# Kernel tuning notes

Hardware: AMD Instinct MI355X
Metric: run time of the kernel (lower is better)

## Reference

```python
import jax, jax.numpy as jnp
import numpy as np

MARGIN = 0.3
LOSS_FLOOR = 1e-06


def setup_inputs() -> dict:
    key = jax.random.key(0)
    k1, k2 = jax.random.split(key)
    embeddings = jax.random.normal(k1, (8192, 128), dtype=jnp.float32)
    labels = jax.random.randint(k2, (8192,), 0, 512, dtype=jnp.int64)
    return {"embeddings": embeddings, "labels": labels}


def _pairwise_dist(x):
    # Euclidean cdist via the GEMM identity; clamp for numerical safety.
    sq = jnp.sum(x * x, axis=1)  # [N]
    d2 = sq[:, None] + sq[None, :] - 2.0 * (x @ x.T)  # [N, N]
    return jnp.sqrt(jnp.maximum(d2, 1e-12))


def reference(embeddings, labels):
    dist = _pairwise_dist(embeddings)  # [N, N]
    same = labels[None, :] == labels[:, None]  # [N, N]
    n = embeddings.shape[0]
    eye = jnp.eye(n, dtype=bool)
    mask_pos = same & ~eye
    mask_neg = ~same  # diagonal is same-label, so already excluded

    neg_inf = jnp.float32(-jnp.inf)
    pos_inf = jnp.float32(jnp.inf)
    hardest_pos = jnp.max(jnp.where(mask_pos, dist, neg_inf), axis=1)  # [N]
    hardest_neg = jnp.min(jnp.where(mask_neg, dist, pos_inf), axis=1)  # [N]

    valid = jnp.any(mask_pos, axis=1) & jnp.any(mask_neg, axis=1)  # [N]
    per_row = jnp.maximum(hardest_pos - hardest_neg + MARGIN, LOSS_FLOOR)
    num_valid = jnp.sum(valid)
    total = jnp.sum(jnp.where(valid, per_row, 0.0))
    return jnp.where(num_valid > 0, total / jnp.maximum(num_valid, 1), 0.0).astype(embeddings.dtype)
```

## Files before the change

kernel.cpp:

```cpp
#include <hip/hip_runtime.h>
#include <math.h>


#define NROWS 8192
#define DIM   128
#define JSPLIT 32
#define JCHUNK (NROWS / JSPLIT)
#define NSUB   4
#define SUBROWS 64

typedef short bf16x8 __attribute__((ext_vector_type(8)));
typedef float f32x4  __attribute__((ext_vector_type(4)));

static __device__ __forceinline__ unsigned short f2bf(float f) {
    unsigned u = __float_as_uint(f);
    unsigned r = (u + 0x7FFFu + ((u >> 16) & 1u)) >> 16;
    return (unsigned short)r;
}

static __device__ __forceinline__ unsigned encf(float f) {
    unsigned u = __float_as_uint(f);
    return (u & 0x80000000u) ? ~u : (u | 0x80000000u);
}
static __device__ __forceinline__ float decf(unsigned e) {
    unsigned u = (e & 0x80000000u) ? (e & 0x7FFFFFFFu) : ~e;
    return __uint_as_float(u);
}
#define ENC_PINF 0xFF800000u
#define ENC_NINF 0x007FFFFFu

static __device__ __forceinline__ void gload_lds16(const void* g, void* l) {
    __builtin_amdgcn_global_load_lds(
        (const __attribute__((address_space(1))) unsigned int*)g,
        (__attribute__((address_space(3))) unsigned int*)l, 16, 0, 0);
}

__global__ __launch_bounds__(256) void prep_kernel(
    const float* __restrict__ x, const int* __restrict__ labels,
    int* __restrict__ hist, float* __restrict__ sqp,
    float* __restrict__ sqh, unsigned* __restrict__ hpE,
    unsigned* __restrict__ hnE, unsigned short* __restrict__ xb) {
    int t = blockIdx.x * 256 + threadIdx.x;
    int row = t >> 5;
    int c = t & 31;
    float4 v = ((const float4*)x)[t];
    float ps = v.x * v.x + v.y * v.y + v.z * v.z + v.w * v.w;
#pragma unroll
    for (int s = 1; s < 32; s <<= 1) ps += __shfl_xor(ps, s, 64);
    if (c == 0) {
        sqp[row] = ps;
        sqh[row] = -0.5f * ps;
        atomicAdd(&hist[labels[row]], 1);
    } else if (c == 1) {
        hpE[row] = ENC_PINF;
    } else if (c == 2) {
        hnE[row] = ENC_NINF;
    }
    ushort4 ob;
    ob.x = f2bf(v.x); ob.y = f2bf(v.y); ob.z = f2bf(v.z); ob.w = f2bf(v.w);
    ((ushort4*)xb)[t] = ob;
}

__global__ __launch_bounds__(256, 4) void pair_kernel(
    const unsigned short* __restrict__ xb, const float* __restrict__ sqh,
    const int* __restrict__ labels,
    unsigned* __restrict__ hpE, unsigned* __restrict__ hnE) {
    __shared__ __attribute__((aligned(16))) unsigned char abuf[2][SUBROWS * 256];
    __shared__ __attribute__((aligned(16))) float sqs[JCHUNK];
    __shared__ __attribute__((aligned(16))) int labs[JCHUNK];

    const int tid = threadIdx.x;
    const int lane = tid & 63;
    const int wid = tid >> 6;
    const int q = lane >> 4;
    const int r = lane & 15;
    const int ibase = blockIdx.x * 256 + wid * 64;
    const int jbase = blockIdx.y * JCHUNK;

    sqs[tid] = sqh[jbase + tid];
    labs[tid] = labels[jbase + tid];

    bf16x8 bfrag[4][4];
    int labi[4];
#pragma unroll
    for (int sub = 0; sub < 4; ++sub) {
        int irow = ibase + sub * 16 + r;
        labi[sub] = labels[irow];
#pragma unroll
        for (int ks = 0; ks < 4; ++ks)
            bfrag[sub][ks] = *(const bf16x8*)(xb + (size_t)irow * DIM + ks * 32 + q * 8);
    }

    float hp[4] = {INFINITY, INFINITY, INFINITY, INFINITY};
    float hn[4] = {-INFINITY, -INFINITY, -INFINITY, -INFINITY};

    auto stage = [&](int s, int buf) {
        const char* gb = (const char*)xb + (size_t)(jbase + s * SUBROWS) * 256;
        unsigned char* lb = &abuf[buf][0];
#pragma unroll
        for (int p = 0; p < 4; ++p) {
            int row = wid * 16 + p * 4 + (lane >> 4);
            int colb = (lane & 15) * 16;
            const void* g = gb + row * 256 + (colb ^ ((row & 15) << 4));
            void* l = lb + wid * 4096 + p * 1024;
            gload_lds16(g, l);
        }
    };

    auto compute_tile = [&](int s, int buf, int t) {
        const unsigned char* lb = &abuf[buf][0];
        const int tt = s * 4 + t;
        bf16x8 af[4];
        const int rowb = (t * 16 + r) * 256;
        const int sw = r << 4;
#pragma unroll
        for (int ks = 0; ks < 4; ++ks)
            af[ks] = *(const bf16x8*)(lb + rowb + ((ks * 64 + q * 16) ^ sw));
        f32x4 ci = *(const f32x4*)(&sqs[tt * 16 + q * 4]);
        int4 labj = *(const int4*)(labs + tt * 16 + q * 4);
#pragma unroll
        for (int sub = 0; sub < 4; ++sub) {
            f32x4 acc = ci;
            acc = __builtin_amdgcn_mfma_f32_16x16x32_bf16(af[0], bfrag[sub][0], acc, 0, 0, 0);
            acc = __builtin_amdgcn_mfma_f32_16x16x32_bf16(af[1], bfrag[sub][1], acc, 0, 0, 0);
            acc = __builtin_amdgcn_mfma_f32_16x16x32_bf16(af[2], bfrag[sub][2], acc, 0, 0, 0);
            acc = __builtin_amdgcn_mfma_f32_16x16x32_bf16(af[3], bfrag[sub][3], acc, 0, 0, 0);
            const int li = labi[sub];
            float u0 = acc[0], u1 = acc[1], u2 = acc[2], u3 = acc[3];
            hp[sub] = fminf(hp[sub], (labj.x == li) ? u0 : INFINITY);
            hn[sub] = fmaxf(hn[sub], (labj.x == li) ? -INFINITY : u0);
            hp[sub] = fminf(hp[sub], (labj.y == li) ? u1 : INFINITY);
            hn[sub] = fmaxf(hn[sub], (labj.y == li) ? -INFINITY : u1);
            hp[sub] = fminf(hp[sub], (labj.z == li) ? u2 : INFINITY);
            hn[sub] = fmaxf(hn[sub], (labj.z == li) ? -INFINITY : u2);
            hp[sub] = fminf(hp[sub], (labj.w == li) ? u3 : INFINITY);
            hn[sub] = fmaxf(hn[sub], (labj.w == li) ? -INFINITY : u3);
        }
    };

    stage(0, 0);
    __syncthreads();
#pragma unroll
    for (int s = 0; s < NSUB; ++s) {
        if (s + 1 < NSUB) stage(s + 1, (s + 1) & 1);
#pragma unroll
        for (int t = 0; t < 4; ++t) compute_tile(s, s & 1, t);
        __syncthreads();
    }

#pragma unroll
    for (int sub = 0; sub < 4; ++sub) {
        hp[sub] = fminf(hp[sub], __shfl_xor(hp[sub], 16, 64));
        hp[sub] = fminf(hp[sub], __shfl_xor(hp[sub], 32, 64));
        hn[sub] = fmaxf(hn[sub], __shfl_xor(hn[sub], 16, 64));
        hn[sub] = fmaxf(hn[sub], __shfl_xor(hn[sub], 32, 64));
    }
    if (lane < 16) {
#pragma unroll
        for (int sub = 0; sub < 4; ++sub) {
            int irow = ibase + sub * 16 + lane;
            atomicMin(&hpE[irow], encf(hp[sub]));
            atomicMax(&hnE[irow], encf(hn[sub]));
        }
    }
}

__global__ __launch_bounds__(256) void reduce_kernel(
    const unsigned* __restrict__ hpE, const unsigned* __restrict__ hnE,
    const float* __restrict__ sqp, const int* __restrict__ labels,
    const int* __restrict__ hist, float* __restrict__ gsum,
    float* __restrict__ gcnt, unsigned* __restrict__ done,
    float* __restrict__ out) {
    int row = blockIdx.x * 256 + threadIdx.x;
    float mnp = decf(hpE[row]);
    float mxn = decf(hnE[row]);
    float s = sqp[row];
    int h = hist[labels[row]];
    float sum = 0.f, cnt = 0.f;
    if (h >= 2 && h < NROWS) {
        float dp = sqrtf(fmaxf(s - 2.f * mnp, 1e-12f));
        float dn = sqrtf(fmaxf(s - 2.f * mxn, 1e-12f));
        sum = fmaxf(dp - dn + 0.3f, 1e-6f);
        cnt = 1.f;
    }
#pragma unroll
    for (int sh = 1; sh < 64; sh <<= 1) {
        sum += __shfl_xor(sum, sh, 64);
        cnt += __shfl_xor(cnt, sh, 64);
    }
    __shared__ float ss[4], sc[4];
    int w = threadIdx.x >> 6;
    if ((threadIdx.x & 63) == 0) { ss[w] = sum; sc[w] = cnt; }
    __syncthreads();
    if (threadIdx.x == 0) {
        atomicAdd(gsum, ss[0] + ss[1] + ss[2] + ss[3]);
        atomicAdd(gcnt, sc[0] + sc[1] + sc[2] + sc[3]);
        __threadfence();
        unsigned t = atomicAdd(done, 1u);
        if (t == gridDim.x - 1) {
            float S = atomicAdd(gsum, 0.f);
            float C = atomicAdd(gcnt, 0.f);
            out[0] = (C > 0.f) ? S / C : 0.f;
        }
    }
}

extern "C" void kernel_launch(void* const* d_in, const int* in_sizes, int n_in,
                              void* d_out, int out_size, void* d_ws, size_t ws_size,
                              hipStream_t stream) {
    const float* x = (const float*)d_in[0];
    const int* labels = (const int*)d_in[1];
    float* out = (float*)d_out;

    char* ws = (char*)d_ws;
    int* hist = (int*)ws;
    float* gsum = (float*)(ws + 2048);
    float* gcnt = (float*)(ws + 2052);
    unsigned* done = (unsigned*)(ws + 2056);
    float* sqp = (float*)(ws + 4096);
    float* sqh = (float*)(ws + 36864);
    unsigned* hpE = (unsigned*)(ws + 69632);
    unsigned* hnE = (unsigned*)(ws + 102400);
    unsigned short* xb = (unsigned short*)(ws + 135168);

    hipMemsetAsync(ws, 0, 4096, stream);
    prep_kernel<<<(NROWS * 32) / 256, 256, 0, stream>>>(
        x, labels, hist, sqp, sqh, hpE, hnE, xb);
    pair_kernel<<<dim3(NROWS / 256, JSPLIT), 256, 0, stream>>>(
        xb, sqh, labels, hpE, hnE);
    reduce_kernel<<<NROWS / 256, 256, 0, stream>>>(
        hpE, hnE, sqp, labels, hist, gsum, gcnt, done, out);
}
```

Baseline: 94.56 us.

## Drop memset and label histogram, double j-split, skip sentinel atomics

Removes the workspace memset by zeroing the global accumulators inside prep_kernel. Replaces the label histogram with a validity test based on whether the per-row extrema remain at their encoded infinity sentinels. Halves the j-chunk size (JSPLIT 64, SUBROWS 32), which doubles the grid, and raises the launch-bounds occupancy hint to 8 blocks. Skips atomics when a block found no positive or negative for a row. Smaller chunks mean more redundant per-block loads of the i-row fragments and more atomic traffic overall.

```diff
diff --git a/kernel.cpp b/kernel.cpp
--- a/kernel.cpp
+++ b/kernel.cpp
@@ -4,10 +4,10 @@
 
 #define NROWS 8192
 #define DIM   128
-#define JSPLIT 32
+#define JSPLIT 64
 #define JCHUNK (NROWS / JSPLIT)
 #define NSUB   4
-#define SUBROWS 64
+#define SUBROWS 32
 
 typedef short bf16x8 __attribute__((ext_vector_type(8)));
 typedef float f32x4  __attribute__((ext_vector_type(4)));
@@ -36,10 +36,11 @@
 }
 
 __global__ __launch_bounds__(256) void prep_kernel(
-    const float* __restrict__ x, const int* __restrict__ labels,
-    int* __restrict__ hist, float* __restrict__ sqp,
+    const float* __restrict__ x, float* __restrict__ sqp,
     float* __restrict__ sqh, unsigned* __restrict__ hpE,
-    unsigned* __restrict__ hnE, unsigned short* __restrict__ xb) {
+    unsigned* __restrict__ hnE, unsigned short* __restrict__ xb,
+    float* __restrict__ gsum, float* __restrict__ gcnt,
+    unsigned* __restrict__ done) {
     int t = blockIdx.x * 256 + threadIdx.x;
     int row = t >> 5;
     int c = t & 31;
@@ -50,18 +51,19 @@
     if (c == 0) {
         sqp[row] = ps;
         sqh[row] = -0.5f * ps;
-        atomicAdd(&hist[labels[row]], 1);
     } else if (c == 1) {
         hpE[row] = ENC_PINF;
     } else if (c == 2) {
         hnE[row] = ENC_NINF;
+    } else if (t == 3) {
+        *gsum = 0.f; *gcnt = 0.f; *done = 0u;
     }
     ushort4 ob;
     ob.x = f2bf(v.x); ob.y = f2bf(v.y); ob.z = f2bf(v.z); ob.w = f2bf(v.w);
     ((ushort4*)xb)[t] = ob;
 }
 
-__global__ __launch_bounds__(256, 4) void pair_kernel(
+__global__ __launch_bounds__(256, 8) void pair_kernel(
     const unsigned short* __restrict__ xb, const float* __restrict__ sqh,
     const int* __restrict__ labels,
     unsigned* __restrict__ hpE, unsigned* __restrict__ hnE) {
@@ -77,8 +79,10 @@
     const int ibase = blockIdx.x * 256 + wid * 64;
     const int jbase = blockIdx.y * JCHUNK;
 
-    sqs[tid] = sqh[jbase + tid];
-    labs[tid] = labels[jbase + tid];
+    if (tid < JCHUNK) {
+        sqs[tid] = sqh[jbase + tid];
+        labs[tid] = labels[jbase + tid];
+    }
 
     bf16x8 bfrag[4][4];
     int labi[4];
@@ -98,18 +102,18 @@
         const char* gb = (const char*)xb + (size_t)(jbase + s * SUBROWS) * 256;
         unsigned char* lb = &abuf[buf][0];
 #pragma unroll
-        for (int p = 0; p < 4; ++p) {
-            int row = wid * 16 + p * 4 + (lane >> 4);
+        for (int p = 0; p < 2; ++p) {
+            int row = wid * 8 + p * 4 + (lane >> 4);
             int colb = (lane & 15) * 16;
             const void* g = gb + row * 256 + (colb ^ ((row & 15) << 4));
-            void* l = lb + wid * 4096 + p * 1024;
+            void* l = lb + wid * 2048 + p * 1024;
             gload_lds16(g, l);
         }
     };
 
     auto compute_tile = [&](int s, int buf, int t) {
         const unsigned char* lb = &abuf[buf][0];
-        const int tt = s * 4 + t;
+        const int tt = s * 2 + t;
         bf16x8 af[4];
         const int rowb = (t * 16 + r) * 256;
         const int sw = r << 4;
@@ -144,7 +148,7 @@
     for (int s = 0; s < NSUB; ++s) {
         if (s + 1 < NSUB) stage(s + 1, (s + 1) & 1);
 #pragma unroll
-        for (int t = 0; t < 4; ++t) compute_tile(s, s & 1, t);
+        for (int t = 0; t < 2; ++t) compute_tile(s, s & 1, t);
         __syncthreads();
     }
 
@@ -159,27 +163,27 @@
 #pragma unroll
         for (int sub = 0; sub < 4; ++sub) {
             int irow = ibase + sub * 16 + lane;
-            atomicMin(&hpE[irow], encf(hp[sub]));
-            atomicMax(&hnE[irow], encf(hn[sub]));
+            unsigned ep = encf(hp[sub]);
+            if (ep != ENC_PINF) atomicMin(&hpE[irow], ep);
+            unsigned en = encf(hn[sub]);
+            if (en != ENC_NINF) atomicMax(&hnE[irow], en);
         }
     }
 }
 
 __global__ __launch_bounds__(256) void reduce_kernel(
     const unsigned* __restrict__ hpE, const unsigned* __restrict__ hnE,
-    const float* __restrict__ sqp, const int* __restrict__ labels,
-    const int* __restrict__ hist, float* __restrict__ gsum,
+    const float* __restrict__ sqp, float* __restrict__ gsum,
     float* __restrict__ gcnt, unsigned* __restrict__ done,
     float* __restrict__ out) {
     int row = blockIdx.x * 256 + threadIdx.x;
-    float mnp = decf(hpE[row]);
-    float mxn = decf(hnE[row]);
+    unsigned hpv = hpE[row];
+    unsigned hnv = hnE[row];
     float s = sqp[row];
-    int h = hist[labels[row]];
     float sum = 0.f, cnt = 0.f;
-    if (h >= 2 && h < NROWS) {
-        float dp = sqrtf(fmaxf(s - 2.f * mnp, 1e-12f));
-        float dn = sqrtf(fmaxf(s - 2.f * mxn, 1e-12f));
+    if (hpv != ENC_PINF && hnv != ENC_NINF) {
+        float dp = sqrtf(fmaxf(s - 2.f * decf(hpv), 1e-12f));
+        float dn = sqrtf(fmaxf(s - 2.f * decf(hnv), 1e-12f));
         sum = fmaxf(dp - dn + 0.3f, 1e-6f);
         cnt = 1.f;
     }
@@ -213,21 +217,19 @@
     float* out = (float*)d_out;
 
     char* ws = (char*)d_ws;
-    int* hist = (int*)ws;
-    float* gsum = (float*)(ws + 2048);
-    float* gcnt = (float*)(ws + 2052);
-    unsigned* done = (unsigned*)(ws + 2056);
+    float* gsum = (float*)ws;
+    float* gcnt = (float*)(ws + 4);
+    unsigned* done = (unsigned*)(ws + 8);
     float* sqp = (float*)(ws + 4096);
     float* sqh = (float*)(ws + 36864);
     unsigned* hpE = (unsigned*)(ws + 69632);
     unsigned* hnE = (unsigned*)(ws + 102400);
     unsigned short* xb = (unsigned short*)(ws + 135168);
 
-    hipMemsetAsync(ws, 0, 4096, stream);
     prep_kernel<<<(NROWS * 32) / 256, 256, 0, stream>>>(
-        x, labels, hist, sqp, sqh, hpE, hnE, xb);
+        x, sqp, sqh, hpE, hnE, xb, gsum, gcnt, done);
     pair_kernel<<<dim3(NROWS / 256, JSPLIT), 256, 0, stream>>>(
         xb, sqh, labels, hpE, hnE);
     reduce_kernel<<<NROWS / 256, 256, 0, stream>>>(
-        hpE, hnE, sqp, labels, hist, gsum, gcnt, done, out);
-}
+        hpE, hnE, sqp, gsum, gcnt, done, out);
+}
```

Result: slower. 231.3 us (+144.6%).
